# Kernel tuning notes

Hardware: AMD Instinct MI355X
Metric: run time of the kernel (lower is better)

## Reference

```python
import jax, jax.numpy as jnp
import numpy as np

N = 100000
E = 1600000
IN_CH = 128
OUT_CH = 128
NUM_REL = 16
NUM_BASES = 8


def setup_inputs() -> dict:
    key = jax.random.key(0)
    k1, k2, k3, k4, k5, k6 = jax.random.split(key, 6)
    x = jax.random.normal(k1, (N, IN_CH), dtype=jnp.float32)
    edge_index = jax.random.randint(k2, (2, E), 0, N, dtype=jnp.int64)
    edge_type = jax.random.randint(k3, (E,), 0, NUM_REL, dtype=jnp.int64)
    # glorot-style init for basis weights (last slot = root weight) and comp
    wscale = np.sqrt(6.0 / (IN_CH + OUT_CH)).astype(np.float32)
    weight = jax.random.uniform(k4, (NUM_BASES + 1, IN_CH, OUT_CH), dtype=jnp.float32,
                                minval=-wscale, maxval=wscale)
    cscale = np.sqrt(6.0 / (NUM_REL + NUM_BASES)).astype(np.float32)
    comp = jax.random.uniform(k5, (NUM_REL, NUM_BASES), dtype=jnp.float32,
                              minval=-cscale, maxval=cscale)
    bias = jnp.zeros((OUT_CH,), dtype=jnp.float32)
    return {"x": x, "weight": weight, "comp": comp, "bias": bias,
            "edge_index": edge_index, "edge_type": edge_type, "num_nodes": N}


def reference(x, weight, comp, bias, edge_index, edge_type, num_nodes):
    """RGCN with basis decomposition, mean aggregation, root weight + bias.

    agg[i, b, :] = (1/deg(i)) * sum_{e: dst(e)=i} comp[etype(e), b] * x[src(e)]
    out = concat_b(agg, x_root) @ weight.reshape(-1, out_ch) + bias
    """
    src = edge_index[0]
    dst = edge_index[1]
    num_bases = comp.shape[1]
    coeff = comp[edge_type]            # [E, B] per-edge basis coefficients
    msg = x[src]                       # [E, in] gathered neighbor features
    # per-basis scatter-add into destination nodes (loop over small fixed B)
    aggs = [jax.ops.segment_sum(msg * coeff[:, b:b + 1], dst, num_segments=num_nodes)
            for b in range(num_bases)]
    agg = jnp.stack(aggs, axis=1)      # [N, B, in]
    # mean normalization by in-degree of destination node
    deg = jax.ops.segment_sum(jnp.ones((src.shape[0],), dtype=x.dtype), dst,
                              num_segments=num_nodes)
    agg = agg / jnp.maximum(deg, 1.0)[:, None, None]
    # [N, (B+1)*in]: bases first, then root features (matches weight layout)
    feat = jnp.concatenate([agg.reshape(num_nodes, -1), x], axis=1)
    out = feat @ weight.reshape(-1, weight.shape[-1]) + bias
    return out
```

## Files before the change

### kernel.cpp

```cpp
#include <hip/hip_runtime.h>
#include <hip/hip_bf16.h>
#include <stdint.h>


#define FPAD 1160
#define SCAT_CH 8192

typedef __attribute__((ext_vector_type(8))) __bf16 bf16x8;
typedef __attribute__((ext_vector_type(4))) float f32x4;

#define RFL(v) __builtin_amdgcn_readfirstlane(v)

__global__ __launch_bounds__(256) void k_prep(const float* __restrict__ x,
                                              __hip_bfloat16* __restrict__ xb, int n4,
                                              const float* __restrict__ W,
                                              __hip_bfloat16* __restrict__ Wf,
                                              const int* __restrict__ dst, int E,
                                              int* __restrict__ bcnt, int NB,
                                              int xbB, int wpB, int hbB) {
    extern __shared__ int sc[];
    int b = blockIdx.x;
    if (b < xbB) {
        int i = b * 256 + threadIdx.x;
        if (i < n4) {
            float4 v = ((const float4*)x)[i];
            __hip_bfloat16 h0 = __float2bfloat16(v.x), h1 = __float2bfloat16(v.y);
            __hip_bfloat16 h2 = __float2bfloat16(v.z), h3 = __float2bfloat16(v.w);
            uint32_t p0 = ((uint32_t)*(uint16_t*)&h1 << 16) | *(uint16_t*)&h0;
            uint32_t p1 = ((uint32_t)*(uint16_t*)&h3 << 16) | *(uint16_t*)&h2;
            ((uint2*)xb)[i] = make_uint2(p0, p1);
        }
    } else if (b < xbB + wpB) {
        int idx = (b - xbB) * 256 + threadIdx.x;
        if (idx < 1152 * 128) {
            int k = idx >> 7, n = idx & 127;
            int kb = k >> 5, hi = (k >> 3) & 3, j = k & 7;
            Wf[((((kb << 2) + hi) << 7 | n) << 3) | j] = __float2bfloat16(W[idx]);
        }
    } else {
        for (int i = threadIdx.x; i < NB; i += 256) sc[i] = 0;
        __syncthreads();
        int hb = b - xbB - wpB;
        int stride = hbB * 256;
        for (int e = hb * 256 + threadIdx.x; e < E; e += stride)
            atomicAdd(&sc[dst[e] >> 7], 1);
        __syncthreads();
        for (int i = threadIdx.x; i < NB; i += 256) {
            int c = sc[i];
            if (c) atomicAdd(&bcnt[i], c);
        }
    }
}

__global__ __launch_bounds__(1024) void k_bscan(const int* __restrict__ bcnt, int NB,
                                                int E, int N,
                                                int* __restrict__ base,
                                                int* __restrict__ cursor,
                                                int* __restrict__ row_ptr) {
    __shared__ int s[1024];
    int t = threadIdx.x;
    int v = (t < NB) ? bcnt[t] : 0;
    s[t] = v;
    __syncthreads();
    for (int off = 1; off < 1024; off <<= 1) {
        int u = (t >= off) ? s[t - off] : 0;
        __syncthreads();
        s[t] += u;
        __syncthreads();
    }
    int excl = (t > 0) ? s[t - 1] : 0;
    if (t < NB) { base[t] = excl; cursor[t] = excl; }
    if (t == 0) { base[NB] = E; row_ptr[N] = E; }
}

__global__ __launch_bounds__(256) void k_bscatter(const int* __restrict__ src,
                                                  const int* __restrict__ dst,
                                                  const int* __restrict__ et,
                                                  int E, int NB,
                                                  int* __restrict__ cursor,
                                                  int* __restrict__ brec) {
    extern __shared__ int sm[];
    int* cnt = sm;
    int* gb  = sm + NB;
    for (int i = threadIdx.x; i < NB; i += 256) cnt[i] = 0;
    __syncthreads();
    int e0 = blockIdx.x * SCAT_CH;
    int e1 = min(e0 + SCAT_CH, E);
    for (int e = e0 + threadIdx.x; e < e1; e += 256)
        atomicAdd(&cnt[dst[e] >> 7], 1);
    __syncthreads();
    for (int i = threadIdx.x; i < NB; i += 256) {
        int c = cnt[i];
        gb[i] = c ? atomicAdd(&cursor[i], c) : 0;
    }
    __syncthreads();
    for (int i = threadIdx.x; i < NB; i += 256) cnt[i] = 0;
    __syncthreads();
    for (int e = e0 + threadIdx.x; e < e1; e += 256) {
        int d = dst[e];
        int bk = d >> 7;
        int off = atomicAdd(&cnt[bk], 1);
        brec[gb[bk] + off] = (src[e] << 11) | ((d & 127) << 4) | (et[e] & 15);
    }
}

__global__ __launch_bounds__(256) void k_bsort(const int* __restrict__ brec,
                                               const int* __restrict__ base,
                                               int N,
                                               int* __restrict__ row_ptr,
                                               int* __restrict__ csr) {
    __shared__ int cnt[128], st[128];
    int b = blockIdx.x;
    int s0 = base[b], s1 = base[b + 1];
    int t = threadIdx.x;
    if (t < 128) cnt[t] = 0;
    __syncthreads();
    for (int i = s0 + t; i < s1; i += 256)
        atomicAdd(&cnt[(brec[i] >> 4) & 127], 1);
    __syncthreads();
    if (t < 128) st[t] = cnt[t];
    __syncthreads();
    for (int off = 1; off < 128; off <<= 1) {
        int u = 0;
        if (t < 128 && t >= off) u = st[t - off];
        __syncthreads();
        if (t < 128) st[t] += u;
        __syncthreads();
    }
    if (t < 128) {
        int excl = st[t] - cnt[t];
        int d = b * 128 + t;
        if (d < N) row_ptr[d] = s0 + excl;
        cnt[t] = excl;
    }
    __syncthreads();
    for (int i = s0 + t; i < s1; i += 256) {
        int r = brec[i];
        int d7 = (r >> 4) & 127;
        int off = atomicAdd(&cnt[d7], 1);
        csr[s0 + off] = ((r >> 11) << 4) | (r & 15);
    }
}

#define GATH(pp) xb32[(uint32_t)((pp) >> 4) * 64u + (uint32_t)lane]

#define CONS1(pp, raw) do {                                               \
    uint32_t _r = (raw);                                                  \
    float _x0 = __uint_as_float(_r << 16);                                \
    float _x1 = __uint_as_float(_r & 0xffff0000u);                        \
    const float* _cf = comp + ((pp) & 15) * 8;                            \
    a[0][0] += _cf[0] * _x0; a[0][1] += _cf[0] * _x1;                     \
    a[1][0] += _cf[1] * _x0; a[1][1] += _cf[1] * _x1;                     \
    a[2][0] += _cf[2] * _x0; a[2][1] += _cf[2] * _x1;                     \
    a[3][0] += _cf[3] * _x0; a[3][1] += _cf[3] * _x1;                     \
    a[4][0] += _cf[4] * _x0; a[4][1] += _cf[4] * _x1;                     \
    a[5][0] += _cf[5] * _x0; a[5][1] += _cf[5] * _x1;                     \
    a[6][0] += _cf[6] * _x0; a[6][1] += _cf[6] * _x1;                     \
    a[7][0] += _cf[7] * _x0; a[7][1] += _cf[7] * _x1;                     \
} while (0)

__global__ __launch_bounds__(512, 6) void k_fused(const __hip_bfloat16* __restrict__ xb,
                                                  const float* __restrict__ comp,
                                                  const int* __restrict__ row_ptr,
                                                  const int* __restrict__ csr,
                                                  const __hip_bfloat16* __restrict__ Wf,
                                                  const float* __restrict__ bias,
                                                  float* __restrict__ out, int M) {
    __shared__ __hip_bfloat16 fl[16][FPAD];
    const uint32_t* __restrict__ xb32 = (const uint32_t*)xb;
    int t = threadIdx.x;
    int wid = t >> 6, lane = t & 63;
    int i0 = blockIdx.x * 16;

    #pragma unroll 1
    for (int rep = 0; rep < 2; rep++) {
        int lr = wid * 2 + rep;
        int iu = RFL(i0 + lr);
        float a[8][2];
        #pragma unroll
        for (int b = 0; b < 8; b++) { a[b][0] = 0.f; a[b][1] = 0.f; }
        int s0 = 0, s1 = 0;
        if (iu < M) {
            s0 = RFL(row_ptr[iu]);
            s1 = RFL(row_ptr[iu + 1]);
        }

        int jj = s0;
        int p0 = RFL(csr[jj]),     p1 = RFL(csr[jj + 1]);
        int p2 = RFL(csr[jj + 2]), p3 = RFL(csr[jj + 3]);
        int p4 = RFL(csr[jj + 4]), p5 = RFL(csr[jj + 5]);
        int p6 = RFL(csr[jj + 6]), p7 = RFL(csr[jj + 7]);
        uint32_t w0 = GATH(p0), w1 = GATH(p1), w2 = GATH(p2), w3 = GATH(p3);
        uint32_t w4 = GATH(p4), w5 = GATH(p5), w6 = GATH(p6), w7 = GATH(p7);
        int q0 = RFL(csr[jj + 8]),  q1 = RFL(csr[jj + 9]);
        int q2 = RFL(csr[jj + 10]), q3 = RFL(csr[jj + 11]);
        int q4 = RFL(csr[jj + 12]), q5 = RFL(csr[jj + 13]);
        int q6 = RFL(csr[jj + 14]), q7 = RFL(csr[jj + 15]);
        uint32_t v0 = GATH(q0), v1 = GATH(q1), v2 = GATH(q2), v3 = GATH(q3);
        uint32_t v4 = GATH(q4), v5 = GATH(q5), v6 = GATH(q6), v7 = GATH(q7);

        #pragma unroll 1
        while (jj + 16 < s1) {
            int r0 = RFL(csr[jj + 16]), r1 = RFL(csr[jj + 17]);
            int r2 = RFL(csr[jj + 18]), r3 = RFL(csr[jj + 19]);
            int r4 = RFL(csr[jj + 20]), r5 = RFL(csr[jj + 21]);
            int r6 = RFL(csr[jj + 22]), r7 = RFL(csr[jj + 23]);
            uint32_t u0 = GATH(r0), u1 = GATH(r1), u2 = GATH(r2), u3 = GATH(r3);
            uint32_t u4 = GATH(r4), u5 = GATH(r5), u6 = GATH(r6), u7 = GATH(r7);
            CONS1(p0, w0); CONS1(p1, w1); CONS1(p2, w2); CONS1(p3, w3);
            CONS1(p4, w4); CONS1(p5, w5); CONS1(p6, w6); CONS1(p7, w7);
            p0 = q0; p1 = q1; p2 = q2; p3 = q3;
            p4 = q4; p5 = q5; p6 = q6; p7 = q7;
            w0 = v0; w1 = v1; w2 = v2; w3 = v3;
            w4 = v4; w5 = v5; w6 = v6; w7 = v7;
            q0 = r0; q1 = r1; q2 = r2; q3 = r3;
            q4 = r4; q5 = r5; q6 = r6; q7 = r7;
            v0 = u0; v1 = u1; v2 = u2; v3 = u3;
            v4 = u4; v5 = u5; v6 = u6; v7 = u7;
            jj += 8;
        }
        CONS1(p0, (jj + 0 < s1) ? w0 : 0u);
        CONS1(p1, (jj + 1 < s1) ? w1 : 0u);
        CONS1(p2, (jj + 2 < s1) ? w2 : 0u);
        CONS1(p3, (jj + 3 < s1) ? w3 : 0u);
        CONS1(p4, (jj + 4 < s1) ? w4 : 0u);
        CONS1(p5, (jj + 5 < s1) ? w5 : 0u);
        CONS1(p6, (jj + 6 < s1) ? w6 : 0u);
        CONS1(p7, (jj + 7 < s1) ? w7 : 0u);
        CONS1(q0, (jj + 8 < s1) ? v0 : 0u);
        CONS1(q1, (jj + 9 < s1) ? v1 : 0u);
        CONS1(q2, (jj + 10 < s1) ? v2 : 0u);
        CONS1(q3, (jj + 11 < s1) ? v3 : 0u);
        CONS1(q4, (jj + 12 < s1) ? v4 : 0u);
        CONS1(q5, (jj + 13 < s1) ? v5 : 0u);
        CONS1(q6, (jj + 14 < s1) ? v6 : 0u);
        CONS1(q7, (jj + 15 < s1) ? v7 : 0u);

        float inv = 1.0f / fmaxf((float)(s1 - s0), 1.0f);
        #pragma unroll
        for (int b = 0; b < 8; b++) {
            __hip_bfloat16 h0 = __float2bfloat16(a[b][0] * inv);
            __hip_bfloat16 h1 = __float2bfloat16(a[b][1] * inv);
            uint32_t pk = ((uint32_t)*(uint16_t*)&h1 << 16) | *(uint16_t*)&h0;
            *(uint32_t*)&fl[lr][b * 128 + lane * 2] = pk;
        }
        uint32_t rr = (iu < M) ? xb32[(uint32_t)iu * 64u + lane] : 0u;
        *(uint32_t*)&fl[lr][1024 + lane * 2] = rr;
    }
    __syncthreads();

    int lo = lane & 15, hi = lane >> 4;
    f32x4 acc = (f32x4){0.f, 0.f, 0.f, 0.f};
    const bf16x8* wv = (const bf16x8*)Wf;
    bf16x8 aC = *(const bf16x8*)&fl[lo][hi * 8];
    bf16x8 bC = wv[(hi << 7) + wid * 16 + lo];
    #pragma unroll 4
    for (int kb = 0; kb < 36; kb++) {
        int kn = (kb < 35) ? kb + 1 : 35;
        bf16x8 aN = *(const bf16x8*)&fl[lo][kn * 32 + hi * 8];
        bf16x8 bN = wv[(((kn << 2) + hi) << 7) + wid * 16 + lo];
        acc = __builtin_amdgcn_mfma_f32_16x16x32_bf16(aC, bC, acc, 0, 0, 0);
        aC = aN; bC = bN;
    }
    float bs = bias[wid * 16 + lo];
    #pragma unroll
    for (int q = 0; q < 4; q++) {
        int row = i0 + hi * 4 + q;
        if (row < M)
            out[(size_t)row * 128 + wid * 16 + lo] = acc[q] + bs;
    }
}

extern "C" void kernel_launch(void* const* d_in, const int* in_sizes, int n_in,
                              void* d_out, int out_size, void* d_ws, size_t ws_size,
                              hipStream_t stream) {
    const float* x      = (const float*)d_in[0];
    const float* weight = (const float*)d_in[1];
    const float* comp   = (const float*)d_in[2];
    const float* bias   = (const float*)d_in[3];
    const int*   eidx   = (const int*)d_in[4];
    const int*   etype  = (const int*)d_in[5];

    int N = in_sizes[0] / 128;
    int E = in_sizes[5];
    const int* srcA = eidx;
    const int* dstA = eidx + E;
    int NB = (N + 127) >> 7;

    uint8_t* ws = (uint8_t*)d_ws;
    size_t off = 0;
    auto take = [&](size_t bytes) -> void* {
        void* p = ws + off;
        off = (off + bytes + 255) & ~(size_t)255;
        return p;
    };
    __hip_bfloat16* xb = (__hip_bfloat16*)take((size_t)N * 128 * sizeof(__hip_bfloat16));
    __hip_bfloat16* Wf = (__hip_bfloat16*)take((size_t)1152 * 128 * sizeof(__hip_bfloat16));
    int* row_ptr = (int*)take((size_t)(N + 1) * sizeof(int));
    int* bcnt    = (int*)take((size_t)NB * sizeof(int));
    int* base    = (int*)take((size_t)(NB + 1) * sizeof(int));
    int* cursor  = (int*)take((size_t)NB * sizeof(int));
    int* brec    = (int*)take((size_t)E * sizeof(int));
    int* csr     = (int*)take((size_t)(E + 24) * sizeof(int));
    (void)ws_size;

    int n4 = N * 128 / 4;
    int xbB = (n4 + 255) / 256;
    int wpB = (1152 * 128 + 255) / 256;
    int hbB = 256;
    int scB = (E + SCAT_CH - 1) / SCAT_CH;

    hipMemsetAsync(bcnt, 0, (size_t)NB * sizeof(int), stream);
    hipMemsetAsync(csr + E, 0, 24 * sizeof(int), stream);
    k_prep<<<xbB + wpB + hbB, 256, NB * sizeof(int), stream>>>(
        x, xb, n4, weight, Wf, dstA, E, bcnt, NB, xbB, wpB, hbB);
    k_bscan<<<1, 1024, 0, stream>>>(bcnt, NB, E, N, base, cursor, row_ptr);
    k_bscatter<<<scB, 256, 2 * NB * sizeof(int), stream>>>(
        srcA, dstA, etype, E, NB, cursor, brec);
    k_bsort<<<NB, 256, 0, stream>>>(brec, base, N, row_ptr, csr);
    k_fused<<<(N + 15) / 16, 512, 0, stream>>>(xb, comp, row_ptr, csr, Wf, bias,
                                               (float*)d_out, N);
}
```

Measured before the change: 202.7 us.

## Dynamically assign rows to waves, vectorize basis FMAs, deepen MFMA prefetch

Each wave now takes destination rows from a shared atomic counter instead of a fixed two rows per wave, which balances uneven in-degrees inside a block. The per-edge basis accumulation moves to two-wide float vectors so the compiler can emit packed FMAs. The MFMA loop now prefetches weights and LDS operands two steps ahead, and the first weight tiles and the bias are loaded before the barrier. The scatter chunk size is also doubled. These changes add LDS atomics and raise register pressure.

```diff
diff --git a/kernel.cpp b/kernel.cpp
--- a/kernel.cpp
+++ b/kernel.cpp
@@ -4,10 +4,11 @@
 
 
 #define FPAD 1160
-#define SCAT_CH 8192
+#define SCAT_CH 16384
 
 typedef __attribute__((ext_vector_type(8))) __bf16 bf16x8;
 typedef __attribute__((ext_vector_type(4))) float f32x4;
+typedef __attribute__((ext_vector_type(2))) float f32x2;
 
 #define RFL(v) __builtin_amdgcn_readfirstlane(v)
 
@@ -148,15 +149,14 @@
     uint32_t _r = (raw);                                                  \
     float _x0 = __uint_as_float(_r << 16);                                \
     float _x1 = __uint_as_float(_r & 0xffff0000u);                        \
-    const float* _cf = comp + ((pp) & 15) * 8;                            \
-    a[0][0] += _cf[0] * _x0; a[0][1] += _cf[0] * _x1;                     \
-    a[1][0] += _cf[1] * _x0; a[1][1] += _cf[1] * _x1;                     \
-    a[2][0] += _cf[2] * _x0; a[2][1] += _cf[2] * _x1;                     \
-    a[3][0] += _cf[3] * _x0; a[3][1] += _cf[3] * _x1;                     \
-    a[4][0] += _cf[4] * _x0; a[4][1] += _cf[4] * _x1;                     \
-    a[5][0] += _cf[5] * _x0; a[5][1] += _cf[5] * _x1;                     \
-    a[6][0] += _cf[6] * _x0; a[6][1] += _cf[6] * _x1;                     \
-    a[7][0] += _cf[7] * _x0; a[7][1] += _cf[7] * _x1;                     \
+    const f32x2* _cf = (const f32x2*)(comp + ((pp) & 15) * 8);            \
+    f32x2 _xx0 = (f32x2){_x0, _x0};                                       \
+    f32x2 _xx1 = (f32x2){_x1, _x1};                                       \
+    f32x2 _c0 = _cf[0], _c1 = _cf[1], _c2 = _cf[2], _c3 = _cf[3];         \
+    a0[0] += _c0 * _xx0; a0[1] += _c1 * _xx0;                             \
+    a0[2] += _c2 * _xx0; a0[3] += _c3 * _xx0;                             \
+    a1[0] += _c0 * _xx1; a1[1] += _c1 * _xx1;                             \
+    a1[2] += _c2 * _xx1; a1[3] += _c3 * _xx1;                             \
 } while (0)
 
 __global__ __launch_bounds__(512, 6) void k_fused(const __hip_bfloat16* __restrict__ xb,
@@ -167,18 +167,24 @@
                                                   const float* __restrict__ bias,
                                                   float* __restrict__ out, int M) {
     __shared__ __hip_bfloat16 fl[16][FPAD];
+    __shared__ int snext;
     const uint32_t* __restrict__ xb32 = (const uint32_t*)xb;
     int t = threadIdx.x;
     int wid = t >> 6, lane = t & 63;
     int i0 = blockIdx.x * 16;
+    if (t == 0) snext = 0;
+    __syncthreads();
 
     #pragma unroll 1
-    for (int rep = 0; rep < 2; rep++) {
-        int lr = wid * 2 + rep;
-        int iu = RFL(i0 + lr);
-        float a[8][2];
+    while (true) {
+        int grab = 0;
+        if (lane == 0) grab = atomicAdd(&snext, 1);
+        int lr = RFL(__shfl(grab, 0));
+        if (lr >= 16) break;
+        int iu = i0 + lr;
+        f32x2 a0[4], a1[4];
         #pragma unroll
-        for (int b = 0; b < 8; b++) { a[b][0] = 0.f; a[b][1] = 0.f; }
+        for (int b = 0; b < 4; b++) { a0[b] = (f32x2){0.f, 0.f}; a1[b] = (f32x2){0.f, 0.f}; }
         int s0 = 0, s1 = 0;
         if (iu < M) {
             s0 = RFL(row_ptr[iu]);
@@ -239,35 +245,41 @@
         float inv = 1.0f / fmaxf((float)(s1 - s0), 1.0f);
         #pragma unroll
         for (int b = 0; b < 8; b++) {
-            __hip_bfloat16 h0 = __float2bfloat16(a[b][0] * inv);
-            __hip_bfloat16 h1 = __float2bfloat16(a[b][1] * inv);
+            __hip_bfloat16 h0 = __float2bfloat16(a0[b >> 1][b & 1] * inv);
+            __hip_bfloat16 h1 = __float2bfloat16(a1[b >> 1][b & 1] * inv);
             uint32_t pk = ((uint32_t)*(uint16_t*)&h1 << 16) | *(uint16_t*)&h0;
             *(uint32_t*)&fl[lr][b * 128 + lane * 2] = pk;
         }
         uint32_t rr = (iu < M) ? xb32[(uint32_t)iu * 64u + lane] : 0u;
         *(uint32_t*)&fl[lr][1024 + lane * 2] = rr;
     }
-    __syncthreads();
 
     int lo = lane & 15, hi = lane >> 4;
+    int wcol = wid * 16 + lo;
+    const bf16x8* wv = (const bf16x8*)Wf;
+    bf16x8 bA = wv[(hi << 7) + wcol];
+    bf16x8 bB = wv[(((1 << 2) + hi) << 7) + wcol];
+    float bs = bias[wcol];
+    __syncthreads();
+
     f32x4 acc = (f32x4){0.f, 0.f, 0.f, 0.f};
-    const bf16x8* wv = (const bf16x8*)Wf;
-    bf16x8 aC = *(const bf16x8*)&fl[lo][hi * 8];
-    bf16x8 bC = wv[(hi << 7) + wid * 16 + lo];
+    bf16x8 aA = *(const bf16x8*)&fl[lo][hi * 8];
+    bf16x8 aB = *(const bf16x8*)&fl[lo][32 + hi * 8];
     #pragma unroll 4
-    for (int kb = 0; kb < 36; kb++) {
-        int kn = (kb < 35) ? kb + 1 : 35;
-        bf16x8 aN = *(const bf16x8*)&fl[lo][kn * 32 + hi * 8];
-        bf16x8 bN = wv[(((kn << 2) + hi) << 7) + wid * 16 + lo];
-        acc = __builtin_amdgcn_mfma_f32_16x16x32_bf16(aC, bC, acc, 0, 0, 0);
-        aC = aN; bC = bN;
-    }
-    float bs = bias[wid * 16 + lo];
+    for (int kb = 0; kb < 34; kb++) {
+        bf16x8 aN = *(const bf16x8*)&fl[lo][(kb + 2) * 32 + hi * 8];
+        bf16x8 bN = wv[((((kb + 2) << 2) + hi) << 7) + wcol];
+        acc = __builtin_amdgcn_mfma_f32_16x16x32_bf16(aA, bA, acc, 0, 0, 0);
+        aA = aB; bA = bB; aB = aN; bB = bN;
+    }
+    acc = __builtin_amdgcn_mfma_f32_16x16x32_bf16(aA, bA, acc, 0, 0, 0);
+    acc = __builtin_amdgcn_mfma_f32_16x16x32_bf16(aB, bB, acc, 0, 0, 0);
+
     #pragma unroll
     for (int q = 0; q < 4; q++) {
         int row = i0 + hi * 4 + q;
         if (row < M)
-            out[(size_t)row * 128 + wid * 16 + lo] = acc[q] + bs;
+            out[(size_t)row * 128 + wcol] = acc[q] + bs;
     }
 }
 
```

Result: slower. 213.4 us (+5.3%).
